# Kernel optimization log

Measured on AMD Instinct MI355X. Metric: run time of the kernel, lower is better.

Reference implementation:

```python
import jax, jax.numpy as jnp
import numpy as np


def conv2d_relu(x, W, b, stride=1):
    # x: NHWC, W: HWIO
    y = jax.lax.conv_general_dilated(x, W, (stride, stride), 'VALID',
                                     dimension_numbers=('NHWC', 'HWIO', 'NHWC'))
    return jax.nn.relu(y + b)


def maxpool_3x3_s2(x):
    return jax.lax.reduce_window(x, -jnp.inf, jax.lax.max,
                                 (1, 3, 3, 1), (1, 2, 2, 1), 'VALID')


def locally_connected_relu(x, W, b, k, stride=1):
    # x: [B, H, W, C]; W: [oh, ow, C*k*k, F]; b: [oh, ow, F]
    # Extract patches -> [B, oh, ow, C*k*k], then per-position GEMM.
    p = jax.lax.conv_general_dilated_patches(
        x, (k, k), (stride, stride), 'VALID',
        dimension_numbers=('NHWC', 'HWIO', 'NHWC'))
    return jax.nn.relu(jnp.einsum('bijp,ijpf->bijf', p, W) + b)


def setup_inputs() -> dict:
    key = jax.random.key(0)
    ks = jax.random.split(key, 16)
    s = 0.02  # small init so relu/sigmoid stay in a sane range
    inp = {
        'inputs': jax.random.normal(ks[0], (32, 152, 152, 3), dtype=jnp.float32),
        'W1': jax.random.normal(ks[1], (11, 11, 3, 32), dtype=jnp.float32) * s,
        'b1': jnp.zeros((32,), jnp.float32),
        'W3': jax.random.normal(ks[2], (9, 9, 32, 16), dtype=jnp.float32) * s,
        'b3': jnp.zeros((16,), jnp.float32),
        'LW4': jax.random.normal(ks[3], (54, 54, 9 * 9 * 16, 16), dtype=jnp.float32) * s,
        'Lb4': jnp.zeros((54, 54, 16), jnp.float32),
        'LW5': jax.random.normal(ks[4], (24, 24, 7 * 7 * 16, 16), dtype=jnp.float32) * s,
        'Lb5': jnp.zeros((24, 24, 16), jnp.float32),
        'LW6': jax.random.normal(ks[5], (20, 20, 5 * 5 * 16, 16), dtype=jnp.float32) * s,
        'Lb6': jnp.zeros((20, 20, 16), jnp.float32),
        'W7': jax.random.normal(ks[6], (6400, 4096), dtype=jnp.float32) * s,
        'b7': jnp.zeros((4096,), jnp.float32),
        'W8': jax.random.normal(ks[7], (4096, 1), dtype=jnp.float32) * s,
        'b8': jnp.zeros((1,), jnp.float32),
    }
    return inp


def reference(inputs, W1, b1, W3, b3, LW4, Lb4, LW5, Lb5, LW6, Lb6, W7, b7, W8, b8):
    x = conv2d_relu(inputs, W1, b1)          # [B,142,142,32]
    x = maxpool_3x3_s2(x)                    # [B,70,70,32]
    x = conv2d_relu(x, W3, b3)               # [B,62,62,16]
    x = locally_connected_relu(x, LW4, Lb4, 9, 1)   # [B,54,54,16]
    x = locally_connected_relu(x, LW5, Lb5, 7, 2)   # [B,24,24,16]
    x = locally_connected_relu(x, LW6, Lb6, 5, 1)   # [B,20,20,16]
    x = x.reshape(x.shape[0], -1)            # [B,6400]
    x = jax.nn.relu(x @ W7 + b7)             # [B,4096]  (Dropout is identity at inference)
    return jax.nn.sigmoid(x @ W8 + b8)       # [B,1]
```

## Files before the change

kernel.cpp:

```cpp
#include <hip/hip_runtime.h>
#include <math.h>

#define DEV_INLINE __device__ __forceinline__

DEV_INLINE float relu_f(float v) { return v > 0.f ? v : 0.f; }

DEV_INLINE void fma4(float4& a, float s, const float4& v) {
    a.x += s * v.x; a.y += s * v.y; a.z += s * v.z; a.w += s * v.w;
}

__global__ __launch_bounds__(256) void k_conv1(
    const float* __restrict__ x, const float* __restrict__ W,
    const float* __restrict__ b, float* __restrict__ y)
{
    __shared__ float sx[26 * 42 * 3];
    __shared__ float swc[11 * 3 * 32];
    const int n   = blockIdx.z;
    const int oh0 = blockIdx.y * 16;
    const int ow0 = blockIdx.x * 32;
    const int tid = threadIdx.x;

    const float* xn = x + (size_t)n * 152 * 152 * 3;
    for (int i = tid; i < 26 * 42 * 3; i += 256) {
        int c = i % 3; int t = i / 3; int col = t % 42; int row = t / 42;
        int r  = oh0 + row; if (r > 151) r = 151;
        int cc = ow0 + col; if (cc > 151) cc = 151;
        sx[i] = xn[(r * 152 + cc) * 3 + c];
    }

    const int ty = tid >> 4, tx = tid & 15;
    float acc[2][32];
#pragma unroll
    for (int p = 0; p < 2; ++p)
#pragma unroll
        for (int j = 0; j < 32; ++j) acc[p][j] = 0.f;

    for (int kh = 0; kh < 11; ++kh) {
        __syncthreads();
        const float4* wsrc = (const float4*)W + kh * 264;
        for (int t = tid; t < 264; t += 256) ((float4*)swc)[t] = wsrc[t];
        __syncthreads();

        const float* sxr = &sx[((ty + kh) * 42 + tx) * 3];
        for (int kw = 0; kw < 11; ++kw) {
#pragma unroll
            for (int ic = 0; ic < 3; ++ic) {
                float x0 = sxr[(kw) * 3 + ic];
                float x1 = sxr[(kw + 16) * 3 + ic];
                const float4* wp4 = (const float4*)&swc[(kw * 3 + ic) * 32];
#pragma unroll
                for (int j4 = 0; j4 < 8; ++j4) {
                    float4 w = wp4[j4];
                    acc[0][j4 * 4 + 0] += x0 * w.x;
                    acc[0][j4 * 4 + 1] += x0 * w.y;
                    acc[0][j4 * 4 + 2] += x0 * w.z;
                    acc[0][j4 * 4 + 3] += x0 * w.w;
                    acc[1][j4 * 4 + 0] += x1 * w.x;
                    acc[1][j4 * 4 + 1] += x1 * w.y;
                    acc[1][j4 * 4 + 2] += x1 * w.z;
                    acc[1][j4 * 4 + 3] += x1 * w.w;
                }
            }
        }
    }

#pragma unroll
    for (int p = 0; p < 2; ++p) {
        int oh = oh0 + ty, ow = ow0 + tx + p * 16;
        if (oh < 142 && ow < 142) {
            float* yp = y + (((size_t)n * 142 + oh) * 142 + ow) * 32;
#pragma unroll
            for (int j = 0; j < 32; ++j) yp[j] = relu_f(acc[p][j] + b[j]);
        }
    }
}

__global__ void k_pool(const float* __restrict__ x, float* __restrict__ y)
{
    int idx = blockIdx.x * 256 + threadIdx.x;
    if (idx >= 32 * 70 * 70 * 8) return;
    int c4 = idx & 7; int t = idx >> 3;
    int pw = t % 70; t /= 70; int ph = t % 70; int n = t / 70;
    const float* xp = x + (((size_t)n * 142 + ph * 2) * 142 + pw * 2) * 32 + c4 * 4;
    float4 m = make_float4(-1e30f, -1e30f, -1e30f, -1e30f);
#pragma unroll
    for (int r = 0; r < 3; ++r) {
#pragma unroll
        for (int cc = 0; cc < 3; ++cc) {
            float4 v = *(const float4*)(xp + ((size_t)r * 142 + cc) * 32);
            m.x = fmaxf(m.x, v.x); m.y = fmaxf(m.y, v.y);
            m.z = fmaxf(m.z, v.z); m.w = fmaxf(m.w, v.w);
        }
    }
    *(float4*)(y + (size_t)idx * 4) = m;
}

__global__ __launch_bounds__(256) void k_conv3(
    const float* __restrict__ x, const float* __restrict__ W,
    const float* __restrict__ bias, float* __restrict__ y)
{
    __shared__ float sw[81 * 8 * 16];
    __shared__ float sx[16 * 40 * 9];
    const int n   = blockIdx.z;
    const int oh0 = blockIdx.y * 8;
    const int ow0 = blockIdx.x * 32;
    const int tid = threadIdx.x;
    const int h   = tid >> 7;
    const int rem = tid & 127;
    const int ty = rem >> 4, tx = rem & 15;
    const float* xn = x + (size_t)n * 70 * 70 * 32;

    float acc[2][8];
#pragma unroll
    for (int p = 0; p < 2; ++p)
#pragma unroll
        for (int j = 0; j < 8; ++j) acc[p][j] = 0.f;

    for (int icc = 0; icc < 4; ++icc) {
        const int ic0 = icc * 8;
        __syncthreads();
        const float4* W4 = (const float4*)W;
        for (int t = tid; t < 2592; t += 256) {
            int oc4 = t & 3; int u = t >> 2; int ic = u & 7; int q = u >> 3;
            ((float4*)sw)[t] = W4[(q * 32 + ic0 + ic) * 4 + oc4];
        }
        for (int t = tid; t < 1280; t += 256) {
            int half = t & 1; int pix = t >> 1; int col = pix % 40; int row = pix / 40;
            int r  = oh0 + row; if (r > 69) r = 69;
            int cc = ow0 + col; if (cc > 69) cc = 69;
            float4 v = *(const float4*)&xn[((size_t)(r * 70 + cc)) * 32 + ic0 + half * 4];
            float* d = &sx[(row * 40 + col) * 9 + half * 4];
            d[0] = v.x; d[1] = v.y; d[2] = v.z; d[3] = v.w;
        }
        __syncthreads();

        for (int kh = 0; kh < 9; ++kh) {
            const float* sxr = &sx[((ty + kh) * 40 + tx) * 9];
            for (int kw = 0; kw < 9; ++kw) {
                const int q = kh * 9 + kw;
#pragma unroll
                for (int ic = 0; ic < 8; ++ic) {
                    float x0 = sxr[(kw) * 9 + ic];
                    float x1 = sxr[(kw + 16) * 9 + ic];
                    const float4* wp4 = (const float4*)&sw[(q * 8 + ic) * 16 + h * 8];
                    float4 w0 = wp4[0];
                    float4 w1 = wp4[1];
                    acc[0][0] += x0 * w0.x; acc[0][1] += x0 * w0.y;
                    acc[0][2] += x0 * w0.z; acc[0][3] += x0 * w0.w;
                    acc[0][4] += x0 * w1.x; acc[0][5] += x0 * w1.y;
                    acc[0][6] += x0 * w1.z; acc[0][7] += x0 * w1.w;
                    acc[1][0] += x1 * w0.x; acc[1][1] += x1 * w0.y;
                    acc[1][2] += x1 * w0.z; acc[1][3] += x1 * w0.w;
                    acc[1][4] += x1 * w1.x; acc[1][5] += x1 * w1.y;
                    acc[1][6] += x1 * w1.z; acc[1][7] += x1 * w1.w;
                }
            }
        }
    }

#pragma unroll
    for (int p = 0; p < 2; ++p) {
        int oh = oh0 + ty, ow = ow0 + tx + p * 16;
        if (oh < 62 && ow < 62) {
            float* yp = y + (((size_t)n * 62 + oh) * 62 + ow) * 16 + h * 8;
            const float* bp = bias + h * 8;
#pragma unroll
            for (int j = 0; j < 8; ++j) yp[j] = relu_f(acc[p][j] + bp[j]);
        }
    }
}

template <int K, int S, int XD, int OD, int GC>
__global__ __launch_bounds__(128) void k_lc(
    const float* __restrict__ x, const float* __restrict__ W,
    const float* __restrict__ bias, float* __restrict__ y)
{
    constexpr int K2     = K * K;
    constexpr int STAGES = 16 / GC;
    constexpr int SPAN4  = GC * K2 * 4;
    __shared__ float sw[GC * K2 * 16];

    const int i = blockIdx.y, j = blockIdx.x;
    const int tid = threadIdx.x;
    const int f4 = tid & 3, b = tid >> 2;

    const float* xb = x + ((size_t)b * XD * XD + (size_t)(i * S) * XD + (j * S)) * 16;
    const float4* wsrc_base = (const float4*)(W + (size_t)(i * OD + j) * (K2 * 16) * 16);

    float4 acc = make_float4(0.f, 0.f, 0.f, 0.f);

    for (int st = 0; st < STAGES; ++st) {
        const int c0 = st * GC;
        __syncthreads();
        const float4* wsrc = wsrc_base + (size_t)c0 * K2 * 4;
        for (int t = tid; t < SPAN4; t += 128)
            ((float4*)sw)[t] = wsrc[t];
        __syncthreads();

        for (int kh = 0; kh < K; ++kh) {
            const float* xrow = xb + (size_t)(kh * XD) * 16 + c0;
            for (int kw = 0; kw < K; ++kw) {
                const int q = kh * K + kw;
                const float* xr = xrow + kw * 16;
#pragma unroll
                for (int cq = 0; cq < GC / 4; ++cq) {
                    const float4 xv = *(const float4*)(xr + cq * 4);
                    const int cb = cq * 4;
                    fma4(acc, xv.x, *(const float4*)&sw[((cb + 0) * K2 + q) * 16 + f4 * 4]);
                    fma4(acc, xv.y, *(const float4*)&sw[((cb + 1) * K2 + q) * 16 + f4 * 4]);
                    fma4(acc, xv.z, *(const float4*)&sw[((cb + 2) * K2 + q) * 16 + f4 * 4]);
                    fma4(acc, xv.w, *(const float4*)&sw[((cb + 3) * K2 + q) * 16 + f4 * 4]);
                }
            }
        }
    }

    const float4 bv = *(const float4*)(bias + ((size_t)i * OD + j) * 16 + f4 * 4);
    acc.x = relu_f(acc.x + bv.x); acc.y = relu_f(acc.y + bv.y);
    acc.z = relu_f(acc.z + bv.z); acc.w = relu_f(acc.w + bv.w);
    *(float4*)(y + (((size_t)b * OD + i) * OD + j) * 16 + f4 * 4) = acc;
}

__global__ __launch_bounds__(256) void k_fc7(
    const float* __restrict__ x, const float* __restrict__ W,
    float* __restrict__ part)
{
    const int o  = blockIdx.x * 256 + threadIdx.x;
    const int k0 = blockIdx.y * 400;
    float acc[32];
#pragma unroll
    for (int b = 0; b < 32; ++b) acc[b] = 0.f;
    const float* wp = W + (size_t)k0 * 4096 + o;
    for (int kk = 0; kk < 400; kk += 2) {
        float w0 = wp[(size_t)kk * 4096];
        float w1 = wp[(size_t)(kk + 1) * 4096];
#pragma unroll
        for (int b = 0; b < 32; ++b) {
            float2 xv = *(const float2*)(x + (size_t)b * 6400 + k0 + kk);
            acc[b] += xv.x * w0 + xv.y * w1;
        }
    }
    float* pp = part + ((size_t)blockIdx.y * 32) * 4096 + o;
#pragma unroll
    for (int b = 0; b < 32; ++b) pp[(size_t)b * 4096] = acc[b];
}

__global__ __launch_bounds__(256) void k_fc8(
    const float* __restrict__ part, const float* __restrict__ b7,
    const float* __restrict__ W8, const float* __restrict__ b8,
    float* __restrict__ out)
{
    const int b = blockIdx.x, tid = threadIdx.x;
    float s = 0.f;
    for (int o = tid; o < 4096; o += 256) {
        float v = b7[o];
#pragma unroll
        for (int kb = 0; kb < 16; ++kb) v += part[((size_t)kb * 32 + b) * 4096 + o];
        v = relu_f(v);
        s += v * W8[o];
    }
#pragma unroll
    for (int off = 32; off > 0; off >>= 1) s += __shfl_down(s, off, 64);
    __shared__ float red[4];
    if ((tid & 63) == 0) red[tid >> 6] = s;
    __syncthreads();
    if (tid == 0) {
        float t = red[0] + red[1] + red[2] + red[3] + b8[0];
        out[b] = 1.f / (1.f + expf(-t));
    }
}

extern "C" void kernel_launch(void* const* d_in, const int* in_sizes, int n_in,
                              void* d_out, int out_size, void* d_ws, size_t ws_size,
                              hipStream_t stream)
{
    (void)in_sizes; (void)n_in; (void)out_size; (void)ws_size;
    const float* x   = (const float*)d_in[0];
    const float* W1  = (const float*)d_in[1];
    const float* b1  = (const float*)d_in[2];
    const float* W3  = (const float*)d_in[3];
    const float* b3  = (const float*)d_in[4];
    const float* LW4 = (const float*)d_in[5];
    const float* Lb4 = (const float*)d_in[6];
    const float* LW5 = (const float*)d_in[7];
    const float* Lb5 = (const float*)d_in[8];
    const float* LW6 = (const float*)d_in[9];
    const float* Lb6 = (const float*)d_in[10];
    const float* W7  = (const float*)d_in[11];
    const float* b7  = (const float*)d_in[12];
    const float* W8  = (const float*)d_in[13];
    const float* b8  = (const float*)d_in[14];
    float* out = (float*)d_out;

    float* ws = (float*)d_ws;
    float* y1 = ws;
    float* y2 = ws + 20647936;
    float* y3 = ws;
    float* y4 = ws + 1968128;
    float* y5 = ws + 3461120;
    float* y6 = ws + 3756032;
    float* p7 = ws + 3960832;

    k_conv1<<<dim3(5, 9, 32), 256, 0, stream>>>(x, W1, b1, y1);
    k_pool<<<dim3(4900), 256, 0, stream>>>(y1, y2);
    k_conv3<<<dim3(2, 8, 32), 256, 0, stream>>>(y2, W3, b3, y3);
    k_lc<9, 1, 62, 54, 4><<<dim3(54, 54), 128, 0, stream>>>(y3, LW4, Lb4, y4);
    k_lc<7, 2, 54, 24, 8><<<dim3(24, 24), 128, 0, stream>>>(y4, LW5, Lb5, y5);
    k_lc<5, 1, 24, 20, 16><<<dim3(20, 20), 128, 0, stream>>>(y5, LW6, Lb6, y6);
    k_fc7<<<dim3(16, 16), 256, 0, stream>>>(y6, W7, p7);
    k_fc8<<<dim3(32), 256, 0, stream>>>(p7, b7, W8, b8, out);
}
```

Before: 1.163 ms.

## Restructure conv1 into channel halves, stage LC activations in LDS, split fc7 K further

conv1 now runs two passes over 16-channel halves, keeps the full half-weight set in shared memory, and reads input straight from global memory instead of staging an input tile. This halves accumulator registers per thread. The locally-connected kernel now stages per-row activation patches for all 32 batch items in shared memory and reads weights directly from global memory, replacing the old scheme of staging weights and reading activations from global. fc7 splits K into 32 chunks instead of 16 to launch more blocks, and fc8 reduces 32 partials, so the partial buffer grows and its traffic doubles.

```diff
diff --git a/kernel.cpp b/kernel.cpp
--- a/kernel.cpp
+++ b/kernel.cpp
@@ -13,64 +13,71 @@
     const float* __restrict__ x, const float* __restrict__ W,
     const float* __restrict__ b, float* __restrict__ y)
 {
-    __shared__ float sx[26 * 42 * 3];
-    __shared__ float swc[11 * 3 * 32];
+    __shared__ float swh[363 * 16];
     const int n   = blockIdx.z;
     const int oh0 = blockIdx.y * 16;
     const int ow0 = blockIdx.x * 32;
     const int tid = threadIdx.x;
+    const int ty = tid >> 4, tx = tid & 15;
 
     const float* xn = x + (size_t)n * 152 * 152 * 3;
-    for (int i = tid; i < 26 * 42 * 3; i += 256) {
-        int c = i % 3; int t = i / 3; int col = t % 42; int row = t / 42;
-        int r  = oh0 + row; if (r > 151) r = 151;
-        int cc = ow0 + col; if (cc > 151) cc = 151;
-        sx[i] = xn[(r * 152 + cc) * 3 + c];
-    }
-
-    const int ty = tid >> 4, tx = tid & 15;
-    float acc[2][32];
-#pragma unroll
-    for (int p = 0; p < 2; ++p)
-#pragma unroll
-        for (int j = 0; j < 32; ++j) acc[p][j] = 0.f;
-
-    for (int kh = 0; kh < 11; ++kh) {
-        __syncthreads();
-        const float4* wsrc = (const float4*)W + kh * 264;
-        for (int t = tid; t < 264; t += 256) ((float4*)swc)[t] = wsrc[t];
-        __syncthreads();
-
-        const float* sxr = &sx[((ty + kh) * 42 + tx) * 3];
-        for (int kw = 0; kw < 11; ++kw) {
-#pragma unroll
-            for (int ic = 0; ic < 3; ++ic) {
-                float x0 = sxr[(kw) * 3 + ic];
-                float x1 = sxr[(kw + 16) * 3 + ic];
-                const float4* wp4 = (const float4*)&swc[(kw * 3 + ic) * 32];
-#pragma unroll
-                for (int j4 = 0; j4 < 8; ++j4) {
-                    float4 w = wp4[j4];
-                    acc[0][j4 * 4 + 0] += x0 * w.x;
-                    acc[0][j4 * 4 + 1] += x0 * w.y;
-                    acc[0][j4 * 4 + 2] += x0 * w.z;
-                    acc[0][j4 * 4 + 3] += x0 * w.w;
-                    acc[1][j4 * 4 + 0] += x1 * w.x;
-                    acc[1][j4 * 4 + 1] += x1 * w.y;
-                    acc[1][j4 * 4 + 2] += x1 * w.z;
-                    acc[1][j4 * 4 + 3] += x1 * w.w;
+    const int oh = oh0 + ty;
+    const int c0 = ow0 + tx;
+    const int c1 = c0 + 16;
+    const int c0c = c0 > 141 ? 141 : c0;
+    const int c1c = c1 > 141 ? 141 : c1;
+
+    for (int h = 0; h < 2; ++h) {
+        __syncthreads();
+        const float4* W4 = (const float4*)W;
+        for (int t = tid; t < 1452; t += 256) {
+            int u4 = t & 3; int q = t >> 2;
+            ((float4*)swh)[t] = W4[q * 8 + h * 4 + u4];
+        }
+        __syncthreads();
+
+        float acc[2][16];
+#pragma unroll
+        for (int p = 0; p < 2; ++p)
+#pragma unroll
+            for (int j = 0; j < 16; ++j) acc[p][j] = 0.f;
+
+        for (int kh = 0; kh < 11; ++kh) {
+            int r = oh + kh; if (r > 151) r = 151;
+            const float* row = xn + (size_t)r * 456;
+            const float* p0 = row + c0c * 3;
+            const float* p1 = row + c1c * 3;
+#pragma unroll
+            for (int kw = 0; kw < 11; ++kw) {
+#pragma unroll
+                for (int ic = 0; ic < 3; ++ic) {
+                    float x0 = p0[kw * 3 + ic];
+                    float x1 = p1[kw * 3 + ic];
+                    const float4* wv = (const float4*)&swh[((kh * 11 + kw) * 3 + ic) * 16];
+#pragma unroll
+                    for (int j4 = 0; j4 < 4; ++j4) {
+                        float4 w = wv[j4];
+                        acc[0][j4 * 4 + 0] += x0 * w.x;
+                        acc[0][j4 * 4 + 1] += x0 * w.y;
+                        acc[0][j4 * 4 + 2] += x0 * w.z;
+                        acc[0][j4 * 4 + 3] += x0 * w.w;
+                        acc[1][j4 * 4 + 0] += x1 * w.x;
+                        acc[1][j4 * 4 + 1] += x1 * w.y;
+                        acc[1][j4 * 4 + 2] += x1 * w.z;
+                        acc[1][j4 * 4 + 3] += x1 * w.w;
+                    }
                 }
             }
         }
-    }
-
-#pragma unroll
-    for (int p = 0; p < 2; ++p) {
-        int oh = oh0 + ty, ow = ow0 + tx + p * 16;
-        if (oh < 142 && ow < 142) {
-            float* yp = y + (((size_t)n * 142 + oh) * 142 + ow) * 32;
-#pragma unroll
-            for (int j = 0; j < 32; ++j) yp[j] = relu_f(acc[p][j] + b[j]);
+
+#pragma unroll
+        for (int p = 0; p < 2; ++p) {
+            int ow = ow0 + tx + p * 16;
+            if (oh < 142 && ow < 142) {
+                float* yp = y + (((size_t)n * 142 + oh) * 142 + ow) * 32 + h * 16;
+#pragma unroll
+                for (int j = 0; j < 16; ++j) yp[j] = relu_f(acc[p][j] + b[h * 16 + j]);
+            }
         }
     }
 }
@@ -170,47 +177,45 @@
     }
 }
 
-template <int K, int S, int XD, int OD, int GC>
+template <int K, int S, int XD, int OD>
 __global__ __launch_bounds__(128) void k_lc(
     const float* __restrict__ x, const float* __restrict__ W,
     const float* __restrict__ bias, float* __restrict__ y)
 {
-    constexpr int K2     = K * K;
-    constexpr int STAGES = 16 / GC;
-    constexpr int SPAN4  = GC * K2 * 4;
-    __shared__ float sw[GC * K2 * 16];
+    constexpr int K2   = K * K;
+    constexpr int RV4  = K * 4;
+    constexpr int BSTR = K * 16 + 4;
+    __shared__ float sx[32 * BSTR];
 
     const int i = blockIdx.y, j = blockIdx.x;
     const int tid = threadIdx.x;
     const int f4 = tid & 3, b = tid >> 2;
 
-    const float* xb = x + ((size_t)b * XD * XD + (size_t)(i * S) * XD + (j * S)) * 16;
-    const float4* wsrc_base = (const float4*)(W + (size_t)(i * OD + j) * (K2 * 16) * 16);
-
+    const float* wp = W + (size_t)(i * OD + j) * (K2 * 16) * 16 + f4 * 4;
     float4 acc = make_float4(0.f, 0.f, 0.f, 0.f);
 
-    for (int st = 0; st < STAGES; ++st) {
-        const int c0 = st * GC;
-        __syncthreads();
-        const float4* wsrc = wsrc_base + (size_t)c0 * K2 * 4;
-        for (int t = tid; t < SPAN4; t += 128)
-            ((float4*)sw)[t] = wsrc[t];
-        __syncthreads();
-
-        for (int kh = 0; kh < K; ++kh) {
-            const float* xrow = xb + (size_t)(kh * XD) * 16 + c0;
-            for (int kw = 0; kw < K; ++kw) {
-                const int q = kh * K + kw;
-                const float* xr = xrow + kw * 16;
-#pragma unroll
-                for (int cq = 0; cq < GC / 4; ++cq) {
-                    const float4 xv = *(const float4*)(xr + cq * 4);
-                    const int cb = cq * 4;
-                    fma4(acc, xv.x, *(const float4*)&sw[((cb + 0) * K2 + q) * 16 + f4 * 4]);
-                    fma4(acc, xv.y, *(const float4*)&sw[((cb + 1) * K2 + q) * 16 + f4 * 4]);
-                    fma4(acc, xv.z, *(const float4*)&sw[((cb + 2) * K2 + q) * 16 + f4 * 4]);
-                    fma4(acc, xv.w, *(const float4*)&sw[((cb + 3) * K2 + q) * 16 + f4 * 4]);
-                }
+    for (int kh = 0; kh < K; ++kh) {
+        __syncthreads();
+        for (int t = tid; t < 32 * RV4; t += 128) {
+            int u = t % RV4; int bb = t / RV4;
+            float4 v = *(const float4*)&x[((((size_t)bb * XD) + (i * S + kh)) * XD + j * S) * 16 + u * 4];
+            *(float4*)&sx[bb * BSTR + u * 4] = v;
+        }
+        __syncthreads();
+
+        const float* xr = &sx[b * BSTR];
+        const float* wk = wp + (kh * K) * 16;
+#pragma unroll
+        for (int kw = 0; kw < K; ++kw) {
+            const float* wq = wk + kw * 16;
+#pragma unroll
+            for (int c4 = 0; c4 < 4; ++c4) {
+                float4 xv = *(const float4*)&xr[kw * 16 + c4 * 4];
+                const float* wc = wq + (size_t)(c4 * 4) * (K2 * 16);
+                fma4(acc, xv.x, *(const float4*)(wc + 0 * K2 * 16));
+                fma4(acc, xv.y, *(const float4*)(wc + 1 * K2 * 16));
+                fma4(acc, xv.z, *(const float4*)(wc + 2 * K2 * 16));
+                fma4(acc, xv.w, *(const float4*)(wc + 3 * K2 * 16));
             }
         }
     }
@@ -226,12 +231,12 @@
     float* __restrict__ part)
 {
     const int o  = blockIdx.x * 256 + threadIdx.x;
-    const int k0 = blockIdx.y * 400;
+    const int k0 = blockIdx.y * 200;
     float acc[32];
 #pragma unroll
     for (int b = 0; b < 32; ++b) acc[b] = 0.f;
     const float* wp = W + (size_t)k0 * 4096 + o;
-    for (int kk = 0; kk < 400; kk += 2) {
+    for (int kk = 0; kk < 200; kk += 2) {
         float w0 = wp[(size_t)kk * 4096];
         float w1 = wp[(size_t)(kk + 1) * 4096];
 #pragma unroll
@@ -255,7 +260,7 @@
     for (int o = tid; o < 4096; o += 256) {
         float v = b7[o];
 #pragma unroll
-        for (int kb = 0; kb < 16; ++kb) v += part[((size_t)kb * 32 + b) * 4096 + o];
+        for (int kb = 0; kb < 32; ++kb) v += part[((size_t)kb * 32 + b) * 4096 + o];
         v = relu_f(v);
         s += v * W8[o];
     }
@@ -304,9 +309,9 @@
     k_conv1<<<dim3(5, 9, 32), 256, 0, stream>>>(x, W1, b1, y1);
     k_pool<<<dim3(4900), 256, 0, stream>>>(y1, y2);
     k_conv3<<<dim3(2, 8, 32), 256, 0, stream>>>(y2, W3, b3, y3);
-    k_lc<9, 1, 62, 54, 4><<<dim3(54, 54), 128, 0, stream>>>(y3, LW4, Lb4, y4);
-    k_lc<7, 2, 54, 24, 8><<<dim3(24, 24), 128, 0, stream>>>(y4, LW5, Lb5, y5);
-    k_lc<5, 1, 24, 20, 16><<<dim3(20, 20), 128, 0, stream>>>(y5, LW6, Lb6, y6);
-    k_fc7<<<dim3(16, 16), 256, 0, stream>>>(y6, W7, p7);
+    k_lc<9, 1, 62, 54><<<dim3(54, 54), 128, 0, stream>>>(y3, LW4, Lb4, y4);
+    k_lc<7, 2, 54, 24><<<dim3(24, 24), 128, 0, stream>>>(y4, LW5, Lb5, y5);
+    k_lc<5, 1, 24, 20><<<dim3(20, 20), 128, 0, stream>>>(y5, LW6, Lb6, y6);
+    k_fc7<<<dim3(16, 32), 256, 0, stream>>>(y6, W7, p7);
     k_fc8<<<dim3(32), 256, 0, stream>>>(p7, b7, W8, b8, out);
 }
```

After: 1.408 ms. 21.0% more time.
